# Kernel optimization log

Hardware: AMD Instinct MI355X
Metric: run time of the kernel (lower is better)

## Reference

```python
import jax, jax.numpy as jnp
import numpy as np

B, T, D, R, V, L, QK, H = 8, 1024, 768, 768, 768, 13, 32, 4
HEAD_DIM = QK // H  # 8
TEMPERATURE = 2.0
LN_EPS = 1e-5


def _layernorm(x, g, b):
    m = jnp.mean(x, axis=-1, keepdims=True)
    v = jnp.mean(jnp.square(x - m), axis=-1, keepdims=True)
    return (x - m) * jax.lax.rsqrt(v + LN_EPS) * g + b


def setup_inputs() -> dict:
    key = jax.random.key(0)
    ks = jax.random.split(key, 14)
    s = 0.02
    return {
        "base_hidden_state": jax.random.normal(ks[0], (B, T, D), jnp.float32),
        "layer_reps": jax.random.normal(ks[1], (L, B, T, R), jnp.float32),
        # per-layer aligner Linear(R -> V)
        "aligner_w": jax.random.normal(ks[2], (L, V, R), jnp.float32) * s,
        "aligner_b": jax.random.normal(ks[3], (L, V), jnp.float32) * s,
        # query LayerNorm(D)
        "qln_g": jnp.ones((D,), jnp.float32),
        "qln_b": jnp.zeros((D,), jnp.float32),
        # kv LayerNorm(V)
        "kvln_g": jnp.ones((V,), jnp.float32),
        "kvln_b": jnp.zeros((V,), jnp.float32),
        # q_proj: D -> QK ; k_proj: V -> QK
        "q_w": jax.random.normal(ks[4], (QK, D), jnp.float32) * s,
        "q_b": jax.random.normal(ks[5], (QK,), jnp.float32) * s,
        "k_w": jax.random.normal(ks[6], (QK, V), jnp.float32) * s,
        "k_b": jax.random.normal(ks[7], (QK,), jnp.float32) * s,
        # out_proj: H*V -> D
        "out_w": jax.random.normal(ks[8], (D, H * V), jnp.float32) * s,
        "out_b": jax.random.normal(ks[9], (D,), jnp.float32) * s,
    }


def reference(base_hidden_state, layer_reps, aligner_w, aligner_b,
              qln_g, qln_b, kvln_g, kvln_b, q_w, q_b, k_w, k_b, out_w, out_b):
    # align_representations: per-layer Linear(R->V), stacked -> (B,T,L,V)
    aligned = jnp.einsum('lbtr,lvr->btlv', layer_reps, aligner_w) + aligner_b  # (B,T,L,V)
    # query: LN of final hidden state (Tq = 1 per token)
    Q = _layernorm(base_hidden_state, qln_g, qln_b)           # (B,T,D)
    # K and V share the same LayerNorm output
    KV = _layernorm(aligned, kvln_g, kvln_b)                  # (B,T,L,V)
    # low-dim projections
    q = jnp.einsum('btd,qd->btq', Q, q_w) + q_b               # (B,T,QK)
    k = jnp.einsum('btlv,qv->btlq', KV, k_w) + k_b            # (B,T,L,QK)
    qh = q.reshape(B, T, H, HEAD_DIM)                         # (B,T,H,hd)
    kh = k.reshape(B, T, L, H, HEAD_DIM)                      # (B,T,L,H,hd)
    scale = HEAD_DIM ** 0.5
    scores = jnp.einsum('bthd,btlhd->bthl', qh, kh) / scale / TEMPERATURE  # (B,T,H,L)
    scores = jnp.where(jnp.isnan(scores), -jnp.inf, scores)
    attn = jax.nn.softmax(scores, axis=-1)                    # (B,T,H,L)
    # V is NOT projected: each head attends over the full-dim values
    out_heads = jnp.einsum('bthl,btlv->bthv', attn, KV)       # (B,T,H,V)
    out = jnp.einsum('bthv,dx->btd', out_heads.reshape(B, T, H * V)[..., None, :].squeeze(-2)[..., None, :].squeeze(-2).reshape(B, T, H * V), out_w.reshape(D, H * V).T.reshape(H * V, D)) if False else out_heads.reshape(B, T, H * V) @ out_w.T + out_b  # (B,T,D)
    return out
```

## Files before the change

### kernel.cpp

```cpp
#include <hip/hip_runtime.h>
#include <stdint.h>

#define NB 8
#define NT 1024
#define ND 768
#define NV 768
#define NL 13
#define MTOK (NB*NT)
#define MROWS (MTOK*NL)

typedef __attribute__((ext_vector_type(8))) short short8;
typedef __attribute__((ext_vector_type(4))) float f32x4;

__device__ __forceinline__ unsigned short f2bf(float f) {
    union { float f; unsigned u; } v; v.f = f;
    unsigned r = v.u + 0x7FFFu + ((v.u >> 16) & 1u);
    return (unsigned short)(r >> 16);
}
__device__ __forceinline__ float bf2f(unsigned short u) {
    union { unsigned u; float f; } v; v.u = ((unsigned)u) << 16;
    return v.f;
}
__device__ __forceinline__ unsigned cvtpk(float lo, float hi) {
    unsigned r;
    asm("v_cvt_pk_bf16_f32 %0, %1, %2" : "=v"(r) : "v"(lo), "v"(hi));
    return r;
}
__device__ __forceinline__ void gload16(const void* g, void* l) {
    __builtin_amdgcn_global_load_lds(
        (const __attribute__((address_space(1))) unsigned int*)g,
        (__attribute__((address_space(3))) unsigned int*)l, 16, 0, 0);
}

__global__ __launch_bounds__(256) void conv_f32_bf16(
    const float* __restrict__ s, unsigned short* __restrict__ d, long n)
{
    long i = ((long)blockIdx.x * 256 + threadIdx.x) * 8;
    long st = (long)gridDim.x * 2048;
    for (; i < n; i += st) {
        float4 a = *(const float4*)(s + i);
        float4 b = *(const float4*)(s + i + 4);
        ushort4 u0, u1;
        u0.x = f2bf(a.x); u0.y = f2bf(a.y); u0.z = f2bf(a.z); u0.w = f2bf(a.w);
        u1.x = f2bf(b.x); u1.y = f2bf(b.y); u1.z = f2bf(b.z); u1.w = f2bf(b.w);
        *(ushort4*)(d + i)     = u0;
        *(ushort4*)(d + i + 4) = u1;
    }
}

__global__ __launch_bounds__(256) void gemm_f32a(
    const float* __restrict__ A, const unsigned short* __restrict__ B,
    const float* __restrict__ biasBase, unsigned short* __restrict__ C,
    int K, long aLS, long bLS, int biasLS, long cLayerOff, long cRowStride)
{
    __shared__ __align__(16) unsigned short lsA[2][128 * 40];
    __shared__ __align__(16) unsigned short lsB[2][4096];

    const int bid = blockIdx.x;
    const int xcd = bid & 7, slot = bid >> 3;
    const int grp = xcd * 104 + slot / 6;
    const int nx  = slot % 6;
    const int l   = grp >> 6;
    const long m0 = (long)(grp & 63) * 128;
    const long n0 = (long)nx * 128;

    const int t = threadIdx.x, lane = t & 63, wave = t >> 6;

    const float* Ab = A + (size_t)l * aLS;
    const unsigned short* Bb = B + (size_t)l * bLS;
    const float* bias = biasBase + (size_t)l * biasLS;

    const int aRow = t >> 3;
    const int aChk = t & 7;
    const int brow = wave * 16 + (lane >> 2);
    const int bchk = (lane & 3) ^ ((lane >> 3) & 3);
    const int dB   = wave * 1024 + lane * 16;

    const int wm = (wave >> 1) * 64;
    const int wn = (wave & 1) * 64;
    const int lr = lane & 15;
    const int g4 = lane >> 4;
    const int kg = g4 * 8;
    const int swzB = ((lr >> 1) & 3) * 8;

    f32x4 acc[4][4];
#pragma unroll
    for (int i = 0; i < 4; i++)
#pragma unroll
        for (int j = 0; j < 4; j++) acc[i][j] = (f32x4){0.f, 0.f, 0.f, 0.f};

    f32x4 areg[4];

    auto LOAD_A = [&](int k0) {
#pragma unroll
        for (int i = 0; i < 4; i++)
            areg[i] = *(const f32x4*)(Ab + (m0 + aRow + i * 32) * (size_t)K + k0 + aChk * 4);
    };
    auto WRITE_A = [&](int buf) {
        unsigned short* la = lsA[buf];
#pragma unroll
        for (int i = 0; i < 4; i++) {
            unsigned u0 = cvtpk(areg[i][0], areg[i][1]);
            unsigned u1 = cvtpk(areg[i][2], areg[i][3]);
            uint2 w; w.x = u0; w.y = u1;
            *(uint2*)&la[(aRow + i * 32) * 40 + aChk * 4] = w;
        }
    };
    auto STAGE_B = [&](int buf, int k0) {
        char* lb = (char*)lsB[buf];
#pragma unroll
        for (int i = 0; i < 2; i++) {
            const char* src = (const char*)(Bb + (n0 + i * 64 + brow) * (size_t)K + k0) + bchk * 16;
            gload16(src, lb + i * 4096 + dB);
        }
    };
    auto COMP = [&](int buf) {
        short8 af[4], bv[4];
        const unsigned short* pa = lsA[buf];
        const unsigned short* pb = lsB[buf];
#pragma unroll
        for (int mi = 0; mi < 4; mi++)
            af[mi] = *(const short8*)&pa[(wm + mi * 16 + lr) * 40 + kg];
#pragma unroll
        for (int ni = 0; ni < 4; ni++)
            bv[ni] = *(const short8*)&pb[(wn + ni * 16 + lr) * 32 + (kg ^ swzB)];
#pragma unroll
        for (int mi = 0; mi < 4; mi++)
#pragma unroll
            for (int ni = 0; ni < 4; ni++)
                acc[mi][ni] = __builtin_amdgcn_mfma_f32_16x16x32_bf16(
                    af[mi], bv[ni], acc[mi][ni], 0, 0, 0);
    };

    LOAD_A(0);
    STAGE_B(0, 0);
    WRITE_A(0);
    __syncthreads();
    int cur = 0;
    const int nst = K >> 5;
    for (int ks = 1; ks < nst; ks++) {
        LOAD_A(ks * 32);
        STAGE_B(cur ^ 1, ks * 32);
        COMP(cur);
        WRITE_A(cur ^ 1);
        __syncthreads();
        cur ^= 1;
    }
    COMP(cur);

#pragma unroll
    for (int ni = 0; ni < 4; ni++) {
        long col = n0 + wn + ni * 16 + lr;
        float bvs = bias[col];
#pragma unroll
        for (int mi = 0; mi < 4; mi++) {
#pragma unroll
            for (int r = 0; r < 4; r++) {
                long grow = m0 + wm + mi * 16 + (lane >> 4) * 4 + r;
                size_t coff = (size_t)grow * cRowStride + (size_t)l * cLayerOff + col;
                C[coff] = f2bf(acc[mi][ni][r] + bvs);
            }
        }
    }
}

__global__ __launch_bounds__(256) void gemm_bf16_nt(
    const unsigned short* __restrict__ A, const unsigned short* __restrict__ B,
    const float* __restrict__ bias, float* __restrict__ C,
    int K, long cRowStride)
{
    __shared__ __align__(16) unsigned short lsA[2][4096];
    __shared__ __align__(16) unsigned short lsB[2][4096];

    const int bid = blockIdx.x;
    const int xcd = bid & 7, slot = bid >> 3;
    const int grp = xcd * 8 + slot / 6;
    const int nx  = slot % 6;
    const long m0 = (long)grp * 128;
    const long n0 = (long)nx * 128;

    const int t = threadIdx.x, lane = t & 63, wave = t >> 6;

    const int brow = wave * 16 + (lane >> 2);
    const int bchk = (lane & 3) ^ ((lane >> 3) & 3);
    const int dA   = wave * 1024 + lane * 16;

    const int wm = (wave >> 1) * 64;
    const int wn = (wave & 1) * 64;
    const int lr = lane & 15;
    const int g4 = lane >> 4;
    const int kg = g4 * 8;
    const int swz = ((lr >> 1) & 3) * 8;

    f32x4 acc[4][4];
#pragma unroll
    for (int i = 0; i < 4; i++)
#pragma unroll
        for (int j = 0; j < 4; j++) acc[i][j] = (f32x4){0.f, 0.f, 0.f, 0.f};

    auto STAGE = [&](int buf, int k0) {
        char* la = (char*)lsA[buf];
        char* lb = (char*)lsB[buf];
#pragma unroll
        for (int i = 0; i < 2; i++) {
            const char* sa = (const char*)(A + (m0 + i * 64 + brow) * (size_t)K + k0) + bchk * 16;
            const char* sb = (const char*)(B + (n0 + i * 64 + brow) * (size_t)K + k0) + bchk * 16;
            gload16(sa, la + i * 4096 + dA);
            gload16(sb, lb + i * 4096 + dA);
        }
    };
    auto COMP = [&](int buf) {
        short8 af[4], bv[4];
        const unsigned short* pa = lsA[buf];
        const unsigned short* pb = lsB[buf];
#pragma unroll
        for (int mi = 0; mi < 4; mi++)
            af[mi] = *(const short8*)&pa[(wm + mi * 16 + lr) * 32 + (kg ^ swz)];
#pragma unroll
        for (int ni = 0; ni < 4; ni++)
            bv[ni] = *(const short8*)&pb[(wn + ni * 16 + lr) * 32 + (kg ^ swz)];
#pragma unroll
        for (int mi = 0; mi < 4; mi++)
#pragma unroll
            for (int ni = 0; ni < 4; ni++)
                acc[mi][ni] = __builtin_amdgcn_mfma_f32_16x16x32_bf16(
                    af[mi], bv[ni], acc[mi][ni], 0, 0, 0);
    };

    STAGE(0, 0);
    __syncthreads();
    int cur = 0;
    const int nst = K >> 5;
    for (int ks = 1; ks < nst; ks++) {
        STAGE(cur ^ 1, ks * 32);
        COMP(cur);
        __syncthreads();
        cur ^= 1;
    }
    COMP(cur);

#pragma unroll
    for (int ni = 0; ni < 4; ni++) {
        long col = n0 + wn + ni * 16 + lr;
        float bvs = bias[col];
#pragma unroll
        for (int mi = 0; mi < 4; mi++) {
#pragma unroll
            for (int r = 0; r < 4; r++) {
                long grow = m0 + wm + mi * 16 + (lane >> 4) * 4 + r;
                C[(size_t)grow * cRowStride + col] = acc[mi][ni][r] + bvs;
            }
        }
    }
}

__global__ __launch_bounds__(256) void wtrans(
    const float* __restrict__ kw, const float* __restrict__ kvg,
    const float* __restrict__ kvb, const float* __restrict__ kbias,
    float* __restrict__ kwp, float* __restrict__ skv, float* __restrict__ ckv)
{
    __shared__ float red[8];
    const int q = blockIdx.x, t = threadIdx.x;
    const int lane = t & 63, wave = t >> 6;
    float s = 0.f, c = 0.f;
    for (int v = t; v < 768; v += 256) {
        float w = kw[q * 768 + v];
        float wp = w * kvg[v];
        kwp[q * 768 + v] = wp;
        s += wp;
        c += w * kvb[v];
    }
#pragma unroll
    for (int off = 1; off < 64; off <<= 1) {
        s += __shfl_xor(s, off);
        c += __shfl_xor(c, off);
    }
    if (lane == 0) { red[wave] = s; red[4 + wave] = c; }
    __syncthreads();
    if (t == 0) {
        skv[q] = red[0] + red[1] + red[2] + red[3];
        ckv[q] = red[4] + red[5] + red[6] + red[7] + kbias[q];
    }
}

__global__ __launch_bounds__(256) void ln_rows_f32(
    const float* __restrict__ src, unsigned short* __restrict__ dst,
    const float* __restrict__ gam, const float* __restrict__ bet)
{
    const int lane = threadIdx.x & 63;
    const int wave = threadIdx.x >> 6;
    const size_t row = (size_t)blockIdx.x * 4 + wave;

    float x[3][4];
    float s = 0.f, sq = 0.f;
#pragma unroll
    for (int i = 0; i < 3; i++) {
        int v = i * 256 + lane * 4;
        float4 f = *(const float4*)(src + row * 768 + v);
        x[i][0] = f.x; x[i][1] = f.y; x[i][2] = f.z; x[i][3] = f.w;
#pragma unroll
        for (int e = 0; e < 4; e++) { s += x[i][e]; sq += x[i][e] * x[i][e]; }
    }
#pragma unroll
    for (int off = 1; off < 64; off <<= 1) {
        s  += __shfl_xor(s, off);
        sq += __shfl_xor(sq, off);
    }
    float mean = s * (1.f / 768.f);
    float var  = sq * (1.f / 768.f) - mean * mean;
    float rs   = rsqrtf(var + 1e-5f);
#pragma unroll
    for (int i = 0; i < 3; i++) {
        int v = i * 256 + lane * 4;
        float4 gg = *(const float4*)(gam + v);
        float4 bb = *(const float4*)(bet + v);
        ushort4 o;
        o.x = f2bf((x[i][0] - mean) * rs * gg.x + bb.x);
        o.y = f2bf((x[i][1] - mean) * rs * gg.y + bb.y);
        o.z = f2bf((x[i][2] - mean) * rs * gg.z + bb.z);
        o.w = f2bf((x[i][3] - mean) * rs * gg.w + bb.w);
        *(ushort4*)(dst + row * 768 + v) = o;
    }
}

__global__ __launch_bounds__(256) void proj32(
    const unsigned short* __restrict__ A, const float* __restrict__ W,
    const float* __restrict__ bias, unsigned short* __restrict__ out)
{
    __shared__ __align__(16) unsigned short lsW[32 * 776];
    __shared__ __align__(16) unsigned short lsA[128 * 40];
    const int t = threadIdx.x;

#pragma unroll
    for (int i = 0; i < 24; i++) {
        int fi = t + i * 256;
        int row = fi / 192;
        int c4  = fi % 192;
        float4 f = *(const float4*)(W + row * 768 + c4 * 4);
        ushort4 u;
        u.x = f2bf(f.x); u.y = f2bf(f.y); u.z = f2bf(f.z); u.w = f2bf(f.w);
        *(ushort4*)&lsW[row * 776 + c4 * 4] = u;
    }

    const size_t m0 = (size_t)blockIdx.x * 128;
    const int lane = t & 63, wave = t >> 6;
    const int wm = wave * 32;
    const int lr = lane & 15, kg = (lane >> 4) * 8;
    const int row_s = t >> 3, c4s = t & 7;

    f32x4 acc[2][2];
#pragma unroll
    for (int i = 0; i < 2; i++)
#pragma unroll
        for (int j = 0; j < 2; j++) acc[i][j] = (f32x4){0.f, 0.f, 0.f, 0.f};

    __syncthreads();

    for (int k0 = 0; k0 < 768; k0 += 32) {
#pragma unroll
        for (int i = 0; i < 4; i++) {
            int row = row_s + 32 * i;
            ushort4 v = *(const ushort4*)(A + (m0 + row) * 768 + k0 + c4s * 4);
            *(ushort4*)&lsA[row * 40 + c4s * 4] = v;
        }
        __syncthreads();
        short8 af[2], bw[2];
#pragma unroll
        for (int mi = 0; mi < 2; mi++)
            af[mi] = *(const short8*)&lsA[(wm + mi * 16 + lr) * 40 + kg];
#pragma unroll
        for (int ni = 0; ni < 2; ni++)
            bw[ni] = *(const short8*)&lsW[(ni * 16 + lr) * 776 + k0 + kg];
#pragma unroll
        for (int mi = 0; mi < 2; mi++)
#pragma unroll
            for (int ni = 0; ni < 2; ni++)
                acc[mi][ni] = __builtin_amdgcn_mfma_f32_16x16x32_bf16(
                    af[mi], bw[ni], acc[mi][ni], 0, 0, 0);
        __syncthreads();
    }

#pragma unroll
    for (int ni = 0; ni < 2; ni++) {
        int col = ni * 16 + lr;
        float bv = bias[col];
#pragma unroll
        for (int mi = 0; mi < 2; mi++) {
#pragma unroll
            for (int r = 0; r < 4; r++) {
                size_t grow = m0 + wm + mi * 16 + (lane >> 4) * 4 + r;
                out[grow * 32 + col] = f2bf(acc[mi][ni][r] + bv);
            }
        }
    }
}

__global__ __launch_bounds__(256) void proj32k_stats(
    const unsigned short* __restrict__ A, const float* __restrict__ W,
    const float* __restrict__ skv, const float* __restrict__ ckv,
    unsigned short* __restrict__ out, float2* __restrict__ st)
{
    __shared__ __align__(16) unsigned short lsW[32 * 776];
    __shared__ __align__(16) unsigned short lsA[128 * 40];
    __shared__ float2 lstat[128];
    const int t = threadIdx.x;

#pragma unroll
    for (int i = 0; i < 24; i++) {
        int fi = t + i * 256;
        int row = fi / 192;
        int c4  = fi % 192;
        float4 f = *(const float4*)(W + row * 768 + c4 * 4);
        ushort4 u;
        u.x = f2bf(f.x); u.y = f2bf(f.y); u.z = f2bf(f.z); u.w = f2bf(f.w);
        *(ushort4*)&lsW[row * 776 + c4 * 4] = u;
    }

    const size_t m0 = (size_t)blockIdx.x * 128;
    const int lane = t & 63, wave = t >> 6;
    const int wm = wave * 32;
    const int lr = lane & 15, kg = (lane >> 4) * 8;
    const int row_s = t >> 3, c4s = t & 7;

    f32x4 acc[2][2];
#pragma unroll
    for (int i = 0; i < 2; i++)
#pragma unroll
        for (int j = 0; j < 2; j++) acc[i][j] = (f32x4){0.f, 0.f, 0.f, 0.f};

    float s_[4] = {0.f, 0.f, 0.f, 0.f}, sq_[4] = {0.f, 0.f, 0.f, 0.f};

    __syncthreads();

    for (int k0 = 0; k0 < 768; k0 += 32) {
#pragma unroll
        for (int i = 0; i < 4; i++) {
            int row = row_s + 32 * i;
            ushort4 v = *(const ushort4*)(A + (m0 + row) * 768 + k0 + c4s * 4);
            *(ushort4*)&lsA[row * 40 + c4s * 4] = v;
            float x0 = bf2f(v.x), x1 = bf2f(v.y), x2 = bf2f(v.z), x3 = bf2f(v.w);
            s_[i]  += x0 + x1 + x2 + x3;
            sq_[i] += x0 * x0 + x1 * x1 + x2 * x2 + x3 * x3;
        }
        __syncthreads();
        short8 af[2], bw[2];
#pragma unroll
        for (int mi = 0; mi < 2; mi++)
            af[mi] = *(const short8*)&lsA[(wm + mi * 16 + lr) * 40 + kg];
#pragma unroll
        for (int ni = 0; ni < 2; ni++)
            bw[ni] = *(const short8*)&lsW[(ni * 16 + lr) * 776 + k0 + kg];
#pragma unroll
        for (int mi = 0; mi < 2; mi++)
#pragma unroll
            for (int ni = 0; ni < 2; ni++)
                acc[mi][ni] = __builtin_amdgcn_mfma_f32_16x16x32_bf16(
                    af[mi], bw[ni], acc[mi][ni], 0, 0, 0);
        __syncthreads();
    }

#pragma unroll
    for (int i = 0; i < 4; i++) {
#pragma unroll
        for (int off = 1; off < 8; off <<= 1) {
            s_[i]  += __shfl_xor(s_[i], off);
            sq_[i] += __shfl_xor(sq_[i], off);
        }
    }
    if (c4s == 0) {
#pragma unroll
        for (int i = 0; i < 4; i++) {
            int row = row_s + 32 * i;
            float mean = s_[i] * (1.f / 768.f);
            float var  = sq_[i] * (1.f / 768.f) - mean * mean;
            float2 sv = make_float2(mean, rsqrtf(var + 1e-5f));
            lstat[row] = sv;
            st[m0 + row] = sv;
        }
    }
    __syncthreads();

#pragma unroll
    for (int ni = 0; ni < 2; ni++) {
        int col = ni * 16 + lr;
        float sk = skv[col], ck = ckv[col];
#pragma unroll
        for (int mi = 0; mi < 2; mi++) {
#pragma unroll
            for (int r = 0; r < 4; r++) {
                int lrow = wm + mi * 16 + (lane >> 4) * 4 + r;
                float2 s2 = lstat[lrow];
                out[(m0 + lrow) * 32 + col] =
                    f2bf(s2.y * (acc[mi][ni][r] - s2.x * sk) + ck);
            }
        }
    }
}

__global__ __launch_bounds__(256) void attn2(
    const unsigned short* __restrict__ qb, const unsigned short* __restrict__ kb,
    const unsigned short* __restrict__ kv, const float2* __restrict__ st,
    const float* __restrict__ gv, const float* __restrict__ bvv,
    unsigned short* __restrict__ oh)
{
    __shared__ float lat[4][4][13];
    __shared__ float latc[4][4];
    const int t = threadIdx.x, lane = t & 63, wave = t >> 6;
    const size_t m = (size_t)blockIdx.x * 4 + wave;

    if (lane < 32) {
        int j = lane;
        float qv = bf2f(qb[m * 32 + j]);
        float p[13];
#pragma unroll
        for (int l = 0; l < 13; l++)
            p[l] = qv * bf2f(kb[(m * 13 + l) * 32 + j]);
#pragma unroll
        for (int off = 1; off < 8; off <<= 1)
#pragma unroll
            for (int l = 0; l < 13; l++) p[l] += __shfl_xor(p[l], off);

        const float sc = 0.17677669529663687f;
        float mx = -1e30f;
#pragma unroll
        for (int l = 0; l < 13; l++) { p[l] *= sc; mx = fmaxf(mx, p[l]); }
        float se = 0.f;
#pragma unroll
        for (int l = 0; l < 13; l++) { p[l] = __expf(p[l] - mx); se += p[l]; }
        float inv = 1.f / se;
        if ((j & 7) == 0) {
            int h = j >> 3;
            float corr = 0.f;
#pragma unroll
            for (int l = 0; l < 13; l++) {
                float2 s_ = st[m * 13 + l];
                float wl = p[l] * inv * s_.y;
                lat[wave][h][l] = wl;
                corr += wl * s_.x;
            }
            latc[wave][h] = corr;
        }
    }
    __syncthreads();

    f32x4 g4v[3], b4[3];
#pragma unroll
    for (int i = 0; i < 3; i++) {
        g4v[i] = *(const f32x4*)(gv + i * 256 + lane * 4);
        b4[i] = *(const f32x4*)(bvv + i * 256 + lane * 4);
    }

    float acc[4][3][4];
#pragma unroll
    for (int h = 0; h < 4; h++)
#pragma unroll
        for (int i = 0; i < 3; i++)
#pragma unroll
            for (int e = 0; e < 4; e++) acc[h][i][e] = 0.f;

    for (int l = 0; l < 13; l++) {
        float al[4];
#pragma unroll
        for (int h = 0; h < 4; h++) al[h] = lat[wave][h][l];
#pragma unroll
        for (int i = 0; i < 3; i++) {
            ushort4 u = *(const ushort4*)(kv + (m * 13 + l) * 768 + i * 256 + lane * 4);
            float xv[4] = {bf2f(u.x), bf2f(u.y), bf2f(u.z), bf2f(u.w)};
#pragma unroll
            for (int h = 0; h < 4; h++)
#pragma unroll
                for (int e = 0; e < 4; e++) acc[h][i][e] += al[h] * xv[e];
        }
    }
#pragma unroll
    for (int h = 0; h < 4; h++) {
        float ch = latc[wave][h];
#pragma unroll
        for (int i = 0; i < 3; i++) {
            ushort4 o;
            o.x = f2bf(g4v[i][0] * (acc[h][i][0] - ch) + b4[i][0]);
            o.y = f2bf(g4v[i][1] * (acc[h][i][1] - ch) + b4[i][1]);
            o.z = f2bf(g4v[i][2] * (acc[h][i][2] - ch) + b4[i][2]);
            o.w = f2bf(g4v[i][3] * (acc[h][i][3] - ch) + b4[i][3]);
            *(ushort4*)(oh + m * 3072 + h * 768 + i * 256 + lane * 4) = o;
        }
    }
}

extern "C" void kernel_launch(void* const* d_in, const int* in_sizes, int n_in,
                              void* d_out, int out_size, void* d_ws, size_t ws_size,
                              hipStream_t stream) {
    const float* base  = (const float*)d_in[0];
    const float* reps  = (const float*)d_in[1];
    const float* aw    = (const float*)d_in[2];
    const float* ab    = (const float*)d_in[3];
    const float* qg    = (const float*)d_in[4];
    const float* qbeta = (const float*)d_in[5];
    const float* kvg   = (const float*)d_in[6];
    const float* kvb   = (const float*)d_in[7];
    const float* qw    = (const float*)d_in[8];
    const float* qbias = (const float*)d_in[9];
    const float* kw    = (const float*)d_in[10];
    const float* kbias = (const float*)d_in[11];
    const float* ow    = (const float*)d_in[12];
    const float* obias = (const float*)d_in[13];
    float* out = (float*)d_out;

    float2* stats = (float2*)d_ws;
    float* kwp = (float*)(stats + MROWS);
    float* skv = kwp + 32 * 768;
    float* ckv = skv + 32;
    unsigned short* aligned = (unsigned short*)(ckv + 32);
    unsigned short* UNION = aligned + (size_t)MROWS * 768;
    unsigned short* kbuf = UNION + (size_t)MTOK * 3072;
    unsigned short* qbuf = kbuf + (size_t)MROWS * 32;
    unsigned short* owb  = qbuf + (size_t)MTOK * 32;

    unsigned short* awb = UNION;

    {
        long n = (long)NL * 768 * 768;
        conv_f32_bf16<<<(int)(n / 8 / 256), 256, 0, stream>>>(aw, awb, n);
        long n2 = (long)768 * 3072;
        conv_f32_bf16<<<(int)(n2 / 8 / 256), 256, 0, stream>>>(ow, owb, n2);
        wtrans<<<32, 256, 0, stream>>>(kw, kvg, kvb, kbias, kwp, skv, ckv);
    }

    gemm_f32a<<<4992, 256, 0, stream>>>(
        reps, awb, ab, aligned,
        768, (long)MTOK * 768, (long)768 * 768, 768,
        768L, (long)NL * 768);

    proj32k_stats<<<MROWS / 128, 256, 0, stream>>>(
        aligned, kwp, skv, ckv, kbuf, stats);

    unsigned short* Qn = UNION;
    ln_rows_f32<<<MTOK / 4, 256, 0, stream>>>(base, Qn, qg, qbeta);
    proj32<<<MTOK / 128, 256, 0, stream>>>(Qn, qw, qbias, qbuf);

    unsigned short* oh = UNION;
    attn2<<<MTOK / 4, 256, 0, stream>>>(qbuf, kbuf, aligned, stats, kvg, kvb, oh);

    gemm_bf16_nt<<<384, 256, 0, stream>>>(oh, owb, obias, out, 3072, 768L);
}
```

Measured before the change: 467.0 us.

## Deepen GEMM software pipelines with explicit waitcnt barriers and fixed K unroll

The aligner GEMM now hardcodes K=768, uses two fp32 A register sets so the global A loads run two stages ahead, and replaces __syncthreads with explicit s_waitcnt vmcnt/lgkmcnt plus raw s_barrier so outstanding loads can stay in flight across the barrier. Both GEMMs precompute their per-thread source pointers instead of recomputing addresses every stage. The output GEMM is restructured to wait on partial vmcnt before computing. The goal is to hide global-load latency behind MFMA work. In exchange the kernel depends on manual waitcnt counts being correct, which risks races, and it uses more registers.

```diff
diff --git a/kernel.cpp b/kernel.cpp
--- a/kernel.cpp
+++ b/kernel.cpp
@@ -31,6 +31,10 @@
         (const __attribute__((address_space(1))) unsigned int*)g,
         (__attribute__((address_space(3))) unsigned int*)l, 16, 0, 0);
 }
+
+#define WAIT4 asm volatile("s_waitcnt vmcnt(4) lgkmcnt(0)" ::: "memory")
+#define WAIT0 asm volatile("s_waitcnt vmcnt(0) lgkmcnt(0)" ::: "memory")
+#define BARR  { __builtin_amdgcn_s_barrier(); __builtin_amdgcn_sched_barrier(0); }
 
 __global__ __launch_bounds__(256) void conv_f32_bf16(
     const float* __restrict__ s, unsigned short* __restrict__ d, long n)
@@ -51,7 +55,7 @@
 __global__ __launch_bounds__(256) void gemm_f32a(
     const float* __restrict__ A, const unsigned short* __restrict__ B,
     const float* __restrict__ biasBase, unsigned short* __restrict__ C,
-    int K, long aLS, long bLS, int biasLS, long cLayerOff, long cRowStride)
+    long aLS, long bLS, int biasLS, long cLayerOff, long cRowStride)
 {
     __shared__ __align__(16) unsigned short lsA[2][128 * 40];
     __shared__ __align__(16) unsigned short lsB[2][4096];
@@ -83,37 +87,32 @@
     const int kg = g4 * 8;
     const int swzB = ((lr >> 1) & 3) * 8;
 
+    const float* aBp[4];
+#pragma unroll
+    for (int i = 0; i < 4; i++)
+        aBp[i] = Ab + (m0 + aRow + i * 32) * (size_t)768 + aChk * 4;
+    const unsigned short* bSp0 = Bb + (n0 + brow) * (size_t)768 + bchk * 8;
+    const unsigned short* bSp1 = Bb + (n0 + 64 + brow) * (size_t)768 + bchk * 8;
+
     f32x4 acc[4][4];
 #pragma unroll
     for (int i = 0; i < 4; i++)
 #pragma unroll
         for (int j = 0; j < 4; j++) acc[i][j] = (f32x4){0.f, 0.f, 0.f, 0.f};
 
-    f32x4 areg[4];
-
-    auto LOAD_A = [&](int k0) {
-#pragma unroll
-        for (int i = 0; i < 4; i++)
-            areg[i] = *(const f32x4*)(Ab + (m0 + aRow + i * 32) * (size_t)K + k0 + aChk * 4);
-    };
-    auto WRITE_A = [&](int buf) {
-        unsigned short* la = lsA[buf];
-#pragma unroll
-        for (int i = 0; i < 4; i++) {
-            unsigned u0 = cvtpk(areg[i][0], areg[i][1]);
-            unsigned u1 = cvtpk(areg[i][2], areg[i][3]);
-            uint2 w; w.x = u0; w.y = u1;
-            *(uint2*)&la[(aRow + i * 32) * 40 + aChk * 4] = w;
-        }
-    };
-    auto STAGE_B = [&](int buf, int k0) {
-        char* lb = (char*)lsB[buf];
-#pragma unroll
-        for (int i = 0; i < 2; i++) {
-            const char* src = (const char*)(Bb + (n0 + i * 64 + brow) * (size_t)K + k0) + bchk * 16;
-            gload16(src, lb + i * 4096 + dB);
-        }
-    };
+    f32x4 ar0[4], ar1[4];
+
+#define LOADA(R, KOFF) { _Pragma("unroll") \
+    for (int i_ = 0; i_ < 4; i_++) (R)[i_] = *(const f32x4*)(aBp[i_] + (KOFF)); }
+#define WRITEA(R, BUF) { unsigned short* la_ = lsA[BUF]; _Pragma("unroll") \
+    for (int i_ = 0; i_ < 4; i_++) { uint2 w_; \
+        w_.x = cvtpk((R)[i_][0], (R)[i_][1]); \
+        w_.y = cvtpk((R)[i_][2], (R)[i_][3]); \
+        *(uint2*)&la_[(aRow + i_ * 32) * 40 + aChk * 4] = w_; } }
+#define STAGEB(BUF, KOFF) { char* lb_ = (char*)lsB[BUF]; \
+    gload16(bSp0 + (KOFF), lb_ + dB); \
+    gload16(bSp1 + (KOFF), lb_ + 4096 + dB); }
+
     auto COMP = [&](int buf) {
         short8 af[4], bv[4];
         const unsigned short* pa = lsA[buf];
@@ -132,21 +131,35 @@
                     af[mi], bv[ni], acc[mi][ni], 0, 0, 0);
     };
 
-    LOAD_A(0);
-    STAGE_B(0, 0);
-    WRITE_A(0);
-    __syncthreads();
-    int cur = 0;
-    const int nst = K >> 5;
-    for (int ks = 1; ks < nst; ks++) {
-        LOAD_A(ks * 32);
-        STAGE_B(cur ^ 1, ks * 32);
-        COMP(cur);
-        WRITE_A(cur ^ 1);
-        __syncthreads();
-        cur ^= 1;
-    }
-    COMP(cur);
+#define GITER(R, KS, DOLOAD, USE4) { \
+    STAGEB((KS) & 1, (KS) * 32); \
+    WRITEA(R, (KS) & 1); \
+    if (DOLOAD) LOADA(R, ((KS) + 2) * 32); \
+    COMP(((KS) - 1) & 1); \
+    if (USE4) { WAIT4; } else { WAIT0; } \
+    BARR; }
+
+    STAGEB(0, 0);
+    LOADA(ar0, 0);
+    WRITEA(ar0, 0);
+    LOADA(ar1, 32);
+    LOADA(ar0, 64);
+    asm volatile("s_waitcnt lgkmcnt(0)" ::: "memory");
+    BARR;
+
+    for (int kp = 1; kp <= 19; kp += 2) {
+        GITER(ar1, kp, 1, 1);
+        GITER(ar0, kp + 1, 1, 1);
+    }
+    GITER(ar1, 21, 1, 1);
+    GITER(ar0, 22, 0, 0);
+    GITER(ar1, 23, 0, 0);
+    COMP(1);
+
+#undef GITER
+#undef STAGEB
+#undef WRITEA
+#undef LOADA
 
 #pragma unroll
     for (int ni = 0; ni < 4; ni++) {
@@ -192,6 +205,11 @@
     const int kg = g4 * 8;
     const int swz = ((lr >> 1) & 3) * 8;
 
+    const unsigned short* aSp0 = A + (m0 + brow) * (size_t)K + bchk * 8;
+    const unsigned short* aSp1 = A + (m0 + 64 + brow) * (size_t)K + bchk * 8;
+    const unsigned short* bSp0 = B + (n0 + brow) * (size_t)K + bchk * 8;
+    const unsigned short* bSp1 = B + (n0 + 64 + brow) * (size_t)K + bchk * 8;
+
     f32x4 acc[4][4];
 #pragma unroll
     for (int i = 0; i < 4; i++)
@@ -201,13 +219,10 @@
     auto STAGE = [&](int buf, int k0) {
         char* la = (char*)lsA[buf];
         char* lb = (char*)lsB[buf];
-#pragma unroll
-        for (int i = 0; i < 2; i++) {
-            const char* sa = (const char*)(A + (m0 + i * 64 + brow) * (size_t)K + k0) + bchk * 16;
-            const char* sb = (const char*)(B + (n0 + i * 64 + brow) * (size_t)K + k0) + bchk * 16;
-            gload16(sa, la + i * 4096 + dA);
-            gload16(sb, lb + i * 4096 + dA);
-        }
+        gload16(aSp0 + k0, la + dA);
+        gload16(aSp1 + k0, la + 4096 + dA);
+        gload16(bSp0 + k0, lb + dA);
+        gload16(bSp1 + k0, lb + 4096 + dA);
     };
     auto COMP = [&](int buf) {
         short8 af[4], bv[4];
@@ -228,16 +243,17 @@
     };
 
     STAGE(0, 0);
-    __syncthreads();
-    int cur = 0;
     const int nst = K >> 5;
     for (int ks = 1; ks < nst; ks++) {
-        STAGE(cur ^ 1, ks * 32);
-        COMP(cur);
-        __syncthreads();
-        cur ^= 1;
-    }
-    COMP(cur);
+        STAGE(ks & 1, ks * 32);
+        asm volatile("s_waitcnt vmcnt(4)" ::: "memory");
+        BARR;
+        COMP((ks - 1) & 1);
+        BARR;
+    }
+    asm volatile("s_waitcnt vmcnt(0)" ::: "memory");
+    BARR;
+    COMP((nst - 1) & 1);
 
 #pragma unroll
     for (int ni = 0; ni < 4; ni++) {
@@ -628,7 +644,7 @@
 
     gemm_f32a<<<4992, 256, 0, stream>>>(
         reps, awb, ab, aligned,
-        768, (long)MTOK * 768, (long)768 * 768, 768,
+        (long)MTOK * 768, (long)768 * 768, 768,
         768L, (long)NL * 768);
 
     proj32k_stats<<<MROWS / 128, 256, 0, stream>>>(
```

After: 482.1 us. +3.2%, slower.

## Double the K-step per pipeline stage in both bf16 GEMM kernels

Applied to the files above, without the earlier changes.

Both GEMMs now stage 64-wide K slices, kept as two 32-wide sub-buffers, per iteration instead of 32. This halves the number of __syncthreads barriers and loop iterations. The fp32-A GEMM also changes A loading so each thread reads a contiguous 32-float half row, uses a padded stride of 44, and hardcodes K=768. The cost is twice the LDS footprint and more registers for the A prefetch, which may reduce occupancy.

```diff
diff --git a/kernel.cpp b/kernel.cpp
--- a/kernel.cpp
+++ b/kernel.cpp
@@ -51,10 +51,10 @@
 __global__ __launch_bounds__(256) void gemm_f32a(
     const float* __restrict__ A, const unsigned short* __restrict__ B,
     const float* __restrict__ biasBase, unsigned short* __restrict__ C,
-    int K, long aLS, long bLS, int biasLS, long cLayerOff, long cRowStride)
-{
-    __shared__ __align__(16) unsigned short lsA[2][128 * 40];
-    __shared__ __align__(16) unsigned short lsB[2][4096];
+    long aLS, long bLS, int biasLS, long cLayerOff, long cRowStride)
+{
+    __shared__ __align__(16) unsigned short lsA[2][2][128 * 44];
+    __shared__ __align__(16) unsigned short lsB[2][2][4096];
 
     const int bid = blockIdx.x;
     const int xcd = bid & 7, slot = bid >> 3;
@@ -70,11 +70,15 @@
     const unsigned short* Bb = B + (size_t)l * bLS;
     const float* bias = biasBase + (size_t)l * biasLS;
 
-    const int aRow = t >> 3;
-    const int aChk = t & 7;
+    const int aRow  = t >> 1;
+    const int aHalf = t & 1;
+    const float* aSrc = Ab + (m0 + aRow) * (size_t)768 + aHalf * 32;
+
     const int brow = wave * 16 + (lane >> 2);
     const int bchk = (lane & 3) ^ ((lane >> 3) & 3);
     const int dB   = wave * 1024 + lane * 16;
+    const unsigned short* bSp0 = Bb + (n0 + brow) * (size_t)768 + bchk * 8;
+    const unsigned short* bSp1 = Bb + (n0 + 64 + brow) * (size_t)768 + bchk * 8;
 
     const int wm = (wave >> 1) * 64;
     const int wn = (wave & 1) * 64;
@@ -89,60 +93,63 @@
 #pragma unroll
         for (int j = 0; j < 4; j++) acc[i][j] = (f32x4){0.f, 0.f, 0.f, 0.f};
 
-    f32x4 areg[4];
-
-    auto LOAD_A = [&](int k0) {
-#pragma unroll
-        for (int i = 0; i < 4; i++)
-            areg[i] = *(const f32x4*)(Ab + (m0 + aRow + i * 32) * (size_t)K + k0 + aChk * 4);
+    f32x4 areg[8];
+
+    auto LOADA = [&](int k0) {
+#pragma unroll
+        for (int i = 0; i < 8; i++)
+            areg[i] = *(const f32x4*)(aSrc + k0 + i * 4);
     };
-    auto WRITE_A = [&](int buf) {
-        unsigned short* la = lsA[buf];
-#pragma unroll
-        for (int i = 0; i < 4; i++) {
-            unsigned u0 = cvtpk(areg[i][0], areg[i][1]);
-            unsigned u1 = cvtpk(areg[i][2], areg[i][3]);
-            uint2 w; w.x = u0; w.y = u1;
-            *(uint2*)&la[(aRow + i * 32) * 40 + aChk * 4] = w;
+    auto WRITEA = [&](int buf) {
+        unsigned short* la = lsA[buf][aHalf];
+#pragma unroll
+        for (int i = 0; i < 8; i++) {
+            uint2 w;
+            w.x = cvtpk(areg[i][0], areg[i][1]);
+            w.y = cvtpk(areg[i][2], areg[i][3]);
+            *(uint2*)&la[aRow * 44 + i * 4] = w;
         }
     };
-    auto STAGE_B = [&](int buf, int k0) {
-        char* lb = (char*)lsB[buf];
-#pragma unroll
-        for (int i = 0; i < 2; i++) {
-            const char* src = (const char*)(Bb + (n0 + i * 64 + brow) * (size_t)K + k0) + bchk * 16;
-            gload16(src, lb + i * 4096 + dB);
+    auto STAGEB = [&](int buf, int k0) {
+#pragma unroll
+        for (int h = 0; h < 2; h++) {
+            char* lb = (char*)lsB[buf][h];
+            gload16(bSp0 + k0 + h * 32, lb + dB);
+            gload16(bSp1 + k0 + h * 32, lb + 4096 + dB);
         }
     };
     auto COMP = [&](int buf) {
-        short8 af[4], bv[4];
-        const unsigned short* pa = lsA[buf];
-        const unsigned short* pb = lsB[buf];
-#pragma unroll
-        for (int mi = 0; mi < 4; mi++)
-            af[mi] = *(const short8*)&pa[(wm + mi * 16 + lr) * 40 + kg];
-#pragma unroll
-        for (int ni = 0; ni < 4; ni++)
-            bv[ni] = *(const short8*)&pb[(wn + ni * 16 + lr) * 32 + (kg ^ swzB)];
-#pragma unroll
-        for (int mi = 0; mi < 4; mi++)
+#pragma unroll
+        for (int kk = 0; kk < 2; kk++) {
+            short8 af[4], bv[4];
+            const unsigned short* pa = lsA[buf][kk];
+            const unsigned short* pb = lsB[buf][kk];
+#pragma unroll
+            for (int mi = 0; mi < 4; mi++)
+                af[mi] = *(const short8*)&pa[(wm + mi * 16 + lr) * 44 + kg];
 #pragma unroll
             for (int ni = 0; ni < 4; ni++)
-                acc[mi][ni] = __builtin_amdgcn_mfma_f32_16x16x32_bf16(
-                    af[mi], bv[ni], acc[mi][ni], 0, 0, 0);
+                bv[ni] = *(const short8*)&pb[(wn + ni * 16 + lr) * 32 + (kg ^ swzB)];
+#pragma unroll
+            for (int mi = 0; mi < 4; mi++)
+#pragma unroll
+                for (int ni = 0; ni < 4; ni++)
+                    acc[mi][ni] = __builtin_amdgcn_mfma_f32_16x16x32_bf16(
+                        af[mi], bv[ni], acc[mi][ni], 0, 0, 0);
+        }
     };
 
-    LOAD_A(0);
-    STAGE_B(0, 0);
-    WRITE_A(0);
+    LOADA(0);
+    STAGEB(0, 0);
+    WRITEA(0);
     __syncthreads();
+
     int cur = 0;
-    const int nst = K >> 5;
-    for (int ks = 1; ks < nst; ks++) {
-        LOAD_A(ks * 32);
-        STAGE_B(cur ^ 1, ks * 32);
+    for (int ks = 1; ks < 12; ks++) {
+        LOADA(ks * 64);
+        STAGEB(cur ^ 1, ks * 64);
         COMP(cur);
-        WRITE_A(cur ^ 1);
+        WRITEA(cur ^ 1);
         __syncthreads();
         cur ^= 1;
     }
@@ -169,8 +176,8 @@
     const float* __restrict__ bias, float* __restrict__ C,
     int K, long cRowStride)
 {
-    __shared__ __align__(16) unsigned short lsA[2][4096];
-    __shared__ __align__(16) unsigned short lsB[2][4096];
+    __shared__ __align__(16) unsigned short lsA[2][2][4096];
+    __shared__ __align__(16) unsigned short lsB[2][2][4096];
 
     const int bid = blockIdx.x;
     const int xcd = bid & 7, slot = bid >> 3;
@@ -192,6 +199,11 @@
     const int kg = g4 * 8;
     const int swz = ((lr >> 1) & 3) * 8;
 
+    const unsigned short* aSp0 = A + (m0 + brow) * (size_t)K + bchk * 8;
+    const unsigned short* aSp1 = A + (m0 + 64 + brow) * (size_t)K + bchk * 8;
+    const unsigned short* bSp0 = B + (n0 + brow) * (size_t)K + bchk * 8;
+    const unsigned short* bSp1 = B + (n0 + 64 + brow) * (size_t)K + bchk * 8;
+
     f32x4 acc[4][4];
 #pragma unroll
     for (int i = 0; i < 4; i++)
@@ -199,40 +211,43 @@
         for (int j = 0; j < 4; j++) acc[i][j] = (f32x4){0.f, 0.f, 0.f, 0.f};
 
     auto STAGE = [&](int buf, int k0) {
-        char* la = (char*)lsA[buf];
-        char* lb = (char*)lsB[buf];
-#pragma unroll
-        for (int i = 0; i < 2; i++) {
-            const char* sa = (const char*)(A + (m0 + i * 64 + brow) * (size_t)K + k0) + bchk * 16;
-            const char* sb = (const char*)(B + (n0 + i * 64 + brow) * (size_t)K + k0) + bchk * 16;
-            gload16(sa, la + i * 4096 + dA);
-            gload16(sb, lb + i * 4096 + dA);
+#pragma unroll
+        for (int h = 0; h < 2; h++) {
+            char* la = (char*)lsA[buf][h];
+            char* lb = (char*)lsB[buf][h];
+            gload16(aSp0 + k0 + h * 32, la + dA);
+            gload16(aSp1 + k0 + h * 32, la + 4096 + dA);
+            gload16(bSp0 + k0 + h * 32, lb + dA);
+            gload16(bSp1 + k0 + h * 32, lb + 4096 + dA);
         }
     };
     auto COMP = [&](int buf) {
-        short8 af[4], bv[4];
-        const unsigned short* pa = lsA[buf];
-        const unsigned short* pb = lsB[buf];
-#pragma unroll
-        for (int mi = 0; mi < 4; mi++)
-            af[mi] = *(const short8*)&pa[(wm + mi * 16 + lr) * 32 + (kg ^ swz)];
-#pragma unroll
-        for (int ni = 0; ni < 4; ni++)
-            bv[ni] = *(const short8*)&pb[(wn + ni * 16 + lr) * 32 + (kg ^ swz)];
-#pragma unroll
-        for (int mi = 0; mi < 4; mi++)
+#pragma unroll
+        for (int kk = 0; kk < 2; kk++) {
+            short8 af[4], bv[4];
+            const unsigned short* pa = lsA[buf][kk];
+            const unsigned short* pb = lsB[buf][kk];
+#pragma unroll
+            for (int mi = 0; mi < 4; mi++)
+                af[mi] = *(const short8*)&pa[(wm + mi * 16 + lr) * 32 + (kg ^ swz)];
 #pragma unroll
             for (int ni = 0; ni < 4; ni++)
-                acc[mi][ni] = __builtin_amdgcn_mfma_f32_16x16x32_bf16(
-                    af[mi], bv[ni], acc[mi][ni], 0, 0, 0);
+                bv[ni] = *(const short8*)&pb[(wn + ni * 16 + lr) * 32 + (kg ^ swz)];
+#pragma unroll
+            for (int mi = 0; mi < 4; mi++)
+#pragma unroll
+                for (int ni = 0; ni < 4; ni++)
+                    acc[mi][ni] = __builtin_amdgcn_mfma_f32_16x16x32_bf16(
+                        af[mi], bv[ni], acc[mi][ni], 0, 0, 0);
+        }
     };
 
     STAGE(0, 0);
     __syncthreads();
     int cur = 0;
-    const int nst = K >> 5;
+    const int nst = K >> 6;
     for (int ks = 1; ks < nst; ks++) {
-        STAGE(cur ^ 1, ks * 32);
+        STAGE(cur ^ 1, ks * 64);
         COMP(cur);
         __syncthreads();
         cur ^= 1;
@@ -628,7 +643,7 @@
 
     gemm_f32a<<<4992, 256, 0, stream>>>(
         reps, awb, ab, aligned,
-        768, (long)MTOK * 768, (long)768 * 768, 768,
+        (long)MTOK * 768, (long)768 * 768, 768,
         768L, (long)NL * 768);
 
     proj32k_stats<<<MROWS / 128, 256, 0, stream>>>(
```

Result: slower. 641.4 us (+37.3%).

## Enlarge aligner GEMM tile to 256x256 with interleaved MFMA scheduling; shrink output GEMM tile

Applied to the files above, without the earlier changes.

The big per-layer aligner GEMM moves from 128x128 tiles with 256 threads to 256x256 tiles with 512 threads. Its K loop is hardcoded to 768 and split into four MFMA phases separated by raw barriers, with prefetch loads interleaved between phases and s_setprio raised around the MFMAs. The goal is more operand reuse per byte loaded and better overlap of global loads with matrix math. The output projection GEMM goes to 64x128 tiles, doubling its grid to 768 blocks for better occupancy across CUs. The risks are higher register pressure from 8x4 accumulators and more barriers per K step.

```diff
diff --git a/kernel.cpp b/kernel.cpp
--- a/kernel.cpp
+++ b/kernel.cpp
@@ -31,6 +31,8 @@
         (const __attribute__((address_space(1))) unsigned int*)g,
         (__attribute__((address_space(3))) unsigned int*)l, 16, 0, 0);
 }
+
+#define BARRAW { __builtin_amdgcn_s_barrier(); __builtin_amdgcn_sched_barrier(0); }
 
 __global__ __launch_bounds__(256) void conv_f32_bf16(
     const float* __restrict__ s, unsigned short* __restrict__ d, long n)
@@ -48,21 +50,21 @@
     }
 }
 
-__global__ __launch_bounds__(256) void gemm_f32a(
+__global__ __launch_bounds__(512, 2) void gemm_f32a(
     const float* __restrict__ A, const unsigned short* __restrict__ B,
     const float* __restrict__ biasBase, unsigned short* __restrict__ C,
-    int K, long aLS, long bLS, int biasLS, long cLayerOff, long cRowStride)
-{
-    __shared__ __align__(16) unsigned short lsA[2][128 * 40];
-    __shared__ __align__(16) unsigned short lsB[2][4096];
+    long aLS, long bLS, int biasLS, long cLayerOff, long cRowStride)
+{
+    __shared__ __align__(16) unsigned short lsA[2][256 * 40];
+    __shared__ __align__(16) unsigned short lsB[2][256 * 32];
 
     const int bid = blockIdx.x;
     const int xcd = bid & 7, slot = bid >> 3;
-    const int grp = xcd * 104 + slot / 6;
-    const int nx  = slot % 6;
-    const int l   = grp >> 6;
-    const long m0 = (long)(grp & 63) * 128;
-    const long n0 = (long)nx * 128;
+    const int grp = xcd * 52 + slot / 3;
+    const int nx  = slot % 3;
+    const int l   = grp >> 5;
+    const long m0 = (long)(grp & 31) * 256;
+    const long n0 = (long)nx * 256;
 
     const int t = threadIdx.x, lane = t & 63, wave = t >> 6;
 
@@ -70,93 +72,105 @@
     const unsigned short* Bb = B + (size_t)l * bLS;
     const float* bias = biasBase + (size_t)l * biasLS;
 
-    const int aRow = t >> 3;
-    const int aChk = t & 7;
-    const int brow = wave * 16 + (lane >> 2);
-    const int bchk = (lane & 3) ^ ((lane >> 3) & 3);
-    const int dB   = wave * 1024 + lane * 16;
-
-    const int wm = (wave >> 1) * 64;
-    const int wn = (wave & 1) * 64;
+    const int aRow  = t >> 1;
+    const int aHalf = t & 1;
+    const float* aSrc = Ab + (m0 + aRow) * (size_t)768 + aHalf * 16;
+
+    const int brow0 = wave * 16 + (lane >> 2);
+    const int bchk  = (lane & 3) ^ ((lane >> 3) & 3);
+    const int dB0   = wave * 1024 + lane * 16;
+    const unsigned short* bSp0 = Bb + (n0 + brow0) * (size_t)768 + bchk * 8;
+    const unsigned short* bSp1 = Bb + (n0 + 128 + brow0) * (size_t)768 + bchk * 8;
+
+    const int wm = (wave >> 2) * 128;
+    const int wn = (wave & 3) * 64;
     const int lr = lane & 15;
     const int g4 = lane >> 4;
     const int kg = g4 * 8;
     const int swzB = ((lr >> 1) & 3) * 8;
 
-    f32x4 acc[4][4];
-#pragma unroll
-    for (int i = 0; i < 4; i++)
+    f32x4 acc[8][4];
+#pragma unroll
+    for (int i = 0; i < 8; i++)
 #pragma unroll
         for (int j = 0; j < 4; j++) acc[i][j] = (f32x4){0.f, 0.f, 0.f, 0.f};
 
     f32x4 areg[4];
 
-    auto LOAD_A = [&](int k0) {
+    auto LOADA = [&](int k0) {
 #pragma unroll
         for (int i = 0; i < 4; i++)
-            areg[i] = *(const f32x4*)(Ab + (m0 + aRow + i * 32) * (size_t)K + k0 + aChk * 4);
+            areg[i] = *(const f32x4*)(aSrc + k0 + i * 4);
     };
-    auto WRITE_A = [&](int buf) {
+    auto WRITEA = [&](int buf) {
         unsigned short* la = lsA[buf];
 #pragma unroll
         for (int i = 0; i < 4; i++) {
-            unsigned u0 = cvtpk(areg[i][0], areg[i][1]);
-            unsigned u1 = cvtpk(areg[i][2], areg[i][3]);
-            uint2 w; w.x = u0; w.y = u1;
-            *(uint2*)&la[(aRow + i * 32) * 40 + aChk * 4] = w;
+            uint2 w;
+            w.x = cvtpk(areg[i][0], areg[i][1]);
+            w.y = cvtpk(areg[i][2], areg[i][3]);
+            *(uint2*)&la[aRow * 40 + aHalf * 16 + i * 4] = w;
         }
     };
-    auto STAGE_B = [&](int buf, int k0) {
+    auto STAGEB = [&](int buf, int k0) {
         char* lb = (char*)lsB[buf];
-#pragma unroll
-        for (int i = 0; i < 2; i++) {
-            const char* src = (const char*)(Bb + (n0 + i * 64 + brow) * (size_t)K + k0) + bchk * 16;
-            gload16(src, lb + i * 4096 + dB);
-        }
+        gload16(bSp0 + k0, lb + dB0);
+        gload16(bSp1 + k0, lb + 8192 + dB0);
     };
-    auto COMP = [&](int buf) {
-        short8 af[4], bv[4];
-        const unsigned short* pa = lsA[buf];
-        const unsigned short* pb = lsB[buf];
-#pragma unroll
-        for (int mi = 0; mi < 4; mi++)
-            af[mi] = *(const short8*)&pa[(wm + mi * 16 + lr) * 40 + kg];
+
+#define MFMA_PAIR(pa_, bv_, p) { \
+    short8 a0_ = *(const short8*)&(pa_)[(wm + (2*(p)) * 16 + lr) * 40 + kg]; \
+    short8 a1_ = *(const short8*)&(pa_)[(wm + (2*(p)+1) * 16 + lr) * 40 + kg]; \
+    __builtin_amdgcn_s_setprio(1); \
+    _Pragma("unroll") \
+    for (int ni_ = 0; ni_ < 4; ni_++) \
+        acc[2*(p)][ni_] = __builtin_amdgcn_mfma_f32_16x16x32_bf16( \
+            a0_, (bv_)[ni_], acc[2*(p)][ni_], 0, 0, 0); \
+    _Pragma("unroll") \
+    for (int ni_ = 0; ni_ < 4; ni_++) \
+        acc[2*(p)+1][ni_] = __builtin_amdgcn_mfma_f32_16x16x32_bf16( \
+            a1_, (bv_)[ni_], acc[2*(p)+1][ni_], 0, 0, 0); \
+    __builtin_amdgcn_s_setprio(0); }
+
+    LOADA(0);
+    STAGEB(0, 0);
+    WRITEA(0);
+    asm volatile("s_waitcnt vmcnt(0) lgkmcnt(0)" ::: "memory");
+    BARRAW;
+
+    for (int ks = 0; ks < 24; ks++) {
+        const int cur = ks & 1;
+        const unsigned short* pa = lsA[cur];
+        const unsigned short* pb = lsB[cur];
+        const bool pf = (ks < 23);
+        if (pf) LOADA((ks + 1) * 32);
+        short8 bv[4];
 #pragma unroll
         for (int ni = 0; ni < 4; ni++)
             bv[ni] = *(const short8*)&pb[(wn + ni * 16 + lr) * 32 + (kg ^ swzB)];
-#pragma unroll
-        for (int mi = 0; mi < 4; mi++)
-#pragma unroll
-            for (int ni = 0; ni < 4; ni++)
-                acc[mi][ni] = __builtin_amdgcn_mfma_f32_16x16x32_bf16(
-                    af[mi], bv[ni], acc[mi][ni], 0, 0, 0);
-    };
-
-    LOAD_A(0);
-    STAGE_B(0, 0);
-    WRITE_A(0);
-    __syncthreads();
-    int cur = 0;
-    const int nst = K >> 5;
-    for (int ks = 1; ks < nst; ks++) {
-        LOAD_A(ks * 32);
-        STAGE_B(cur ^ 1, ks * 32);
-        COMP(cur);
-        WRITE_A(cur ^ 1);
-        __syncthreads();
-        cur ^= 1;
-    }
-    COMP(cur);
+        MFMA_PAIR(pa, bv, 0);
+        BARRAW;
+        if (pf) STAGEB(cur ^ 1, (ks + 1) * 32);
+        MFMA_PAIR(pa, bv, 1);
+        BARRAW;
+        if (pf) WRITEA(cur ^ 1);
+        MFMA_PAIR(pa, bv, 2);
+        BARRAW;
+        MFMA_PAIR(pa, bv, 3);
+        asm volatile("s_waitcnt vmcnt(0) lgkmcnt(0)" ::: "memory");
+        BARRAW;
+    }
+#undef MFMA_PAIR
 
 #pragma unroll
     for (int ni = 0; ni < 4; ni++) {
         long col = n0 + wn + ni * 16 + lr;
         float bvs = bias[col];
 #pragma unroll
-        for (int mi = 0; mi < 4; mi++) {
+        for (int mi = 0; mi < 8; mi++) {
 #pragma unroll
             for (int r = 0; r < 4; r++) {
-                long grow = m0 + wm + mi * 16 + (lane >> 4) * 4 + r;
+                long grow = m0 + wm + mi * 16 + g4 * 4 + r;
                 size_t coff = (size_t)grow * cRowStride + (size_t)l * cLayerOff + col;
                 C[coff] = f2bf(acc[mi][ni][r] + bvs);
             }
@@ -169,58 +183,58 @@
     const float* __restrict__ bias, float* __restrict__ C,
     int K, long cRowStride)
 {
-    __shared__ __align__(16) unsigned short lsA[2][4096];
-    __shared__ __align__(16) unsigned short lsB[2][4096];
+    __shared__ __align__(16) unsigned short lsA[2][64 * 32];
+    __shared__ __align__(16) unsigned short lsB[2][128 * 32];
 
     const int bid = blockIdx.x;
     const int xcd = bid & 7, slot = bid >> 3;
-    const int grp = xcd * 8 + slot / 6;
+    const int grp = xcd * 16 + slot / 6;
     const int nx  = slot % 6;
-    const long m0 = (long)grp * 128;
+    const long m0 = (long)grp * 64;
     const long n0 = (long)nx * 128;
 
     const int t = threadIdx.x, lane = t & 63, wave = t >> 6;
 
-    const int brow = wave * 16 + (lane >> 2);
-    const int bchk = (lane & 3) ^ ((lane >> 3) & 3);
-    const int dA   = wave * 1024 + lane * 16;
-
-    const int wm = (wave >> 1) * 64;
+    const int srow = wave * 16 + (lane >> 2);
+    const int schk = (lane & 3) ^ ((lane >> 3) & 3);
+    const int dS   = wave * 1024 + lane * 16;
+
+    const int wm = (wave >> 1) * 32;
     const int wn = (wave & 1) * 64;
     const int lr = lane & 15;
     const int g4 = lane >> 4;
     const int kg = g4 * 8;
     const int swz = ((lr >> 1) & 3) * 8;
 
-    f32x4 acc[4][4];
-#pragma unroll
-    for (int i = 0; i < 4; i++)
+    const unsigned short* aSp  = A + (m0 + srow) * (size_t)K + schk * 8;
+    const unsigned short* bSp0 = B + (n0 + srow) * (size_t)K + schk * 8;
+    const unsigned short* bSp1 = B + (n0 + 64 + srow) * (size_t)K + schk * 8;
+
+    f32x4 acc[2][4];
+#pragma unroll
+    for (int i = 0; i < 2; i++)
 #pragma unroll
         for (int j = 0; j < 4; j++) acc[i][j] = (f32x4){0.f, 0.f, 0.f, 0.f};
 
     auto STAGE = [&](int buf, int k0) {
         char* la = (char*)lsA[buf];
         char* lb = (char*)lsB[buf];
-#pragma unroll
-        for (int i = 0; i < 2; i++) {
-            const char* sa = (const char*)(A + (m0 + i * 64 + brow) * (size_t)K + k0) + bchk * 16;
-            const char* sb = (const char*)(B + (n0 + i * 64 + brow) * (size_t)K + k0) + bchk * 16;
-            gload16(sa, la + i * 4096 + dA);
-            gload16(sb, lb + i * 4096 + dA);
-        }
+        gload16(aSp + k0, la + dS);
+        gload16(bSp0 + k0, lb + dS);
+        gload16(bSp1 + k0, lb + 4096 + dS);
     };
     auto COMP = [&](int buf) {
-        short8 af[4], bv[4];
+        short8 af[2], bv[4];
         const unsigned short* pa = lsA[buf];
         const unsigned short* pb = lsB[buf];
 #pragma unroll
-        for (int mi = 0; mi < 4; mi++)
+        for (int mi = 0; mi < 2; mi++)
             af[mi] = *(const short8*)&pa[(wm + mi * 16 + lr) * 32 + (kg ^ swz)];
 #pragma unroll
         for (int ni = 0; ni < 4; ni++)
             bv[ni] = *(const short8*)&pb[(wn + ni * 16 + lr) * 32 + (kg ^ swz)];
 #pragma unroll
-        for (int mi = 0; mi < 4; mi++)
+        for (int mi = 0; mi < 2; mi++)
 #pragma unroll
             for (int ni = 0; ni < 4; ni++)
                 acc[mi][ni] = __builtin_amdgcn_mfma_f32_16x16x32_bf16(
@@ -244,10 +258,10 @@
         long col = n0 + wn + ni * 16 + lr;
         float bvs = bias[col];
 #pragma unroll
-        for (int mi = 0; mi < 4; mi++) {
+        for (int mi = 0; mi < 2; mi++) {
 #pragma unroll
             for (int r = 0; r < 4; r++) {
-                long grow = m0 + wm + mi * 16 + (lane >> 4) * 4 + r;
+                long grow = m0 + wm + mi * 16 + g4 * 4 + r;
                 C[(size_t)grow * cRowStride + col] = acc[mi][ni][r] + bvs;
             }
         }
@@ -626,9 +640,9 @@
         wtrans<<<32, 256, 0, stream>>>(kw, kvg, kvb, kbias, kwp, skv, ckv);
     }
 
-    gemm_f32a<<<4992, 256, 0, stream>>>(
+    gemm_f32a<<<1248, 512, 0, stream>>>(
         reps, awb, ab, aligned,
-        768, (long)MTOK * 768, (long)768 * 768, 768,
+        (long)MTOK * 768, (long)768 * 768, 768,
         768L, (long)NL * 768);
 
     proj32k_stats<<<MROWS / 128, 256, 0, stream>>>(
@@ -641,5 +655,5 @@
     unsigned short* oh = UNION;
     attn2<<<MTOK / 4, 256, 0, stream>>>(qbuf, kbuf, aligned, stats, kvg, kvb, oh);
 
-    gemm_bf16_nt<<<384, 256, 0, stream>>>(oh, owb, obias, out, 3072, 768L);
-}
+    gemm_bf16_nt<<<768, 256, 0, stream>>>(oh, owb, obias, out, 3072, 768L);
+}
```

Result: no change. 462.2 us (-1.0%).
